# Optimization experiments

Measured on AMD Instinct MI355X. Metric: run time of the kernel, lower is better.

The kernel has to match this reference:

```python
import jax, jax.numpy as jnp
import numpy as np

B, QL, CTX, H = 1, 2048, 2048, 4096
NH, NKV, HD = 32, 8, 128


def rotate_half(x):
    x1, x2 = jnp.split(x, 2, axis=-1)
    return jnp.concatenate([-x2, x1], axis=-1)


def apply_rotary(x, cos, sin):
    # x: [B, h, S, HD]; cos/sin: [B, S, HD] -> broadcast over heads
    cos = cos[:, None, :, :]
    sin = sin[:, None, :, :]
    return x * cos + rotate_half(x) * sin


def setup_inputs() -> dict:
    key = jax.random.key(0)
    ks = jax.random.split(key, 8)
    s = 0.02
    return {
        "hidden_states": jax.random.normal(ks[0], (B, QL, H), jnp.float32),
        "target_hidden": jax.random.normal(ks[1], (B, CTX, H), jnp.float32),
        "cos": jax.random.uniform(ks[2], (B, CTX + QL, HD), jnp.float32),
        "sin": jax.random.uniform(ks[3], (B, CTX + QL, HD), jnp.float32),
        "Wq": jax.random.normal(ks[4], (NH * HD, H), jnp.float32) * s,
        "Wk": jax.random.normal(ks[5], (NKV * HD, H), jnp.float32) * s,
        "Wv": jax.random.normal(ks[6], (NKV * HD, H), jnp.float32) * s,
        "Wo": jax.random.normal(ks[7], (H, NH * HD), jnp.float32) * s,
    }


def reference(hidden_states, target_hidden, cos, sin, Wq, Wk, Wv, Wo):
    bsz, q_len, _ = hidden_states.shape
    ctx_len = target_hidden.shape[1]

    def proj(x, W, nh):  # [B,S,H] @ W.T -> [B,nh,S,HD]
        y = jnp.einsum("bsh,dh->bsd", x, W)
        return y.reshape(bsz, x.shape[1], nh, HD).transpose(0, 2, 1, 3)

    q = proj(hidden_states, Wq, NH)
    k_ctx = proj(target_hidden, Wk, NKV)
    v_ctx = proj(target_hidden, Wv, NKV)
    k_noise = proj(hidden_states, Wk, NKV)
    v_noise = proj(hidden_states, Wv, NKV)

    cos_n = cos[:, ctx_len:ctx_len + q_len]
    sin_n = sin[:, ctx_len:ctx_len + q_len]
    q = apply_rotary(q, cos_n, sin_n)
    k_noise = apply_rotary(k_noise, cos_n, sin_n)
    k_ctx = apply_rotary(k_ctx, cos[:, :ctx_len], sin[:, :ctx_len])

    k = jnp.concatenate([k_ctx, k_noise], axis=2)  # [B,NKV,CTX+QL,HD]
    v = jnp.concatenate([v_ctx, v_noise], axis=2)

    n_rep = NH // NKV
    k = jnp.repeat(k, n_rep, axis=1)  # repeat_interleave on head dim
    v = jnp.repeat(v, n_rep, axis=1)

    scale = 1.0 / jnp.sqrt(jnp.asarray(HD, q.dtype))
    scores = jnp.einsum("bhqd,bhkd->bhqk", q, k) * scale
    probs = jax.nn.softmax(scores, axis=-1)
    attn = jnp.einsum("bhqk,bhkd->bhqd", probs, v)
    attn = attn.transpose(0, 2, 1, 3).reshape(bsz, q_len, NH * HD)
    return jnp.einsum("bsd,hd->bsh", attn, Wo)
```

## Files before the change

### kernel.cpp

```cpp
#include <hip/hip_runtime.h>

typedef unsigned short u16;
typedef _Float16 f16;
typedef _Float16 f16x4 __attribute__((ext_vector_type(4)));
typedef _Float16 f16x8 __attribute__((ext_vector_type(8)));
typedef float f32x4 __attribute__((ext_vector_type(4)));

#define GLL16(gptr, lptr)                                                        \
  __builtin_amdgcn_global_load_lds(                                              \
      (const __attribute__((address_space(1))) void*)(gptr),                     \
      (__attribute__((address_space(3))) void*)(lptr), 16, 0, 0)

__global__ void cast_all_k(const float* __restrict__ h, const float* __restrict__ t,
                           const float* __restrict__ wq, const float* __restrict__ wk,
                           const float* __restrict__ wv, const float* __restrict__ wo,
                           f16* __restrict__ Xcat, f16* __restrict__ Wqb,
                           f16* __restrict__ Wkvb, f16* __restrict__ Wob) {
  long i = (long)blockIdx.x * 256 + threadIdx.x;
  const float* s; f16* d; long off;
  if (i < 2097152)        { s = h;  d = Xcat;            off = i; }
  else if (i < 4194304)   { s = t;  d = Xcat + 8388608;  off = i - 2097152; }
  else if (i < 8388608)   { s = wq; d = Wqb;             off = i - 4194304; }
  else if (i < 9437184)   { s = wk; d = Wkvb;            off = i - 8388608; }
  else if (i < 10485760)  { s = wv; d = Wkvb + 4194304;  off = i - 9437184; }
  else                    { s = wo; d = Wob;             off = i - 10485760; }
  float4 v = *(const float4*)(s + off * 4);
  f16x4 o;
  o.x = (f16)v.x; o.y = (f16)v.y; o.z = (f16)v.z; o.w = (f16)v.w;
  *(f16x4*)(d + off * 4) = o;
}

template <int MODE>
__global__ __launch_bounds__(512, 2) void gemm8k(
    const f16* __restrict__ Xcat, const f16* __restrict__ Wqb,
    const f16* __restrict__ Wkvb, const float* __restrict__ cosT,
    const float* __restrict__ sinT, f16* __restrict__ Qb, f16* __restrict__ Kb,
    f16* __restrict__ Vt, const f16* __restrict__ Ao,
    const f16* __restrict__ Wob, float* __restrict__ Cp, float qscale) {
  __shared__ __align__(16) f16 lds[65536];
  const int tid = threadIdx.x;
  const int w = tid >> 6, lane = tid & 63;
  const int quad = lane >> 4, l16 = lane & 15;
  const int wm = w >> 1, wn = w & 1;

  int b = (int)blockIdx.x;
  int l = ((b & 7) << 5) | (b >> 3);

  const f16 *A, *B;
  long tM, tN;
  int NT, kbeg;
  bool isQ = false, isV = false;
  float* Cz = nullptr;
  if (MODE == 0) {
    kbeg = 0; NT = 64;
    if (l < 128) {
      A = Xcat; B = Wqb; tM = (long)(l >> 4) * 256; tN = (long)(l & 15) * 256;
      isQ = true;
    } else {
      int l2 = l - 128;
      A = Xcat; B = Wkvb; tM = (long)(l2 >> 3) * 256; tN = (long)(l2 & 7) * 256;
      isV = (tN >= 1024);
    }
  } else {
    int z = l >> 7, r0 = l & 127;
    A = Ao; B = Wob; tM = (long)(r0 >> 4) * 256; tN = (long)(r0 & 15) * 256;
    kbeg = z * 2048; NT = 32; Cz = Cp + (long)z * 8388608;
  }

  const int sr8 = lane >> 3;
  const int cg = (lane & 7) ^ sr8;
  const f16* Ag = A + (tM + 16 * w + sr8) * 4096 + kbeg + cg * 8;
  const f16* Bg = B + (tN + 16 * w + sr8) * 4096 + kbeg + cg * 8;
  const int ldsw = w * 1024;

#define STAGE_A(hf, t, c)                                                      \
  do {                                                                         \
    const f16* g_ = Ag + (long)(t) * 64 + (long)(hf) * (128 * 4096);           \
    f16* d_ = &lds[(c) * 16384 + (hf) * 8192 + ldsw];                          \
    GLL16(g_, d_);                                                             \
    GLL16(g_ + 8 * 4096, d_ + 512);                                            \
  } while (0)
#define STAGE_B(hf, t, c)                                                      \
  do {                                                                         \
    const f16* g_ = Bg + (long)(t) * 64 + (long)(hf) * (128 * 4096);           \
    f16* d_ = &lds[32768 + (c) * 16384 + (hf) * 8192 + ldsw];                  \
    GLL16(g_, d_);                                                             \
    GLL16(g_ + 8 * 4096, d_ + 512);                                            \
  } while (0)

  const int rA = wm * 64 + l16;
  const int rB = wn * 128 + l16;
  const int sw = l16 & 7;
#define LDA(fr, mi, kk, c)                                                     \
  fr = *(const f16x8*)&lds[(c) * 16384 + (rA + (mi) * 16) * 64 +               \
                           (((kk) * 4 + quad) ^ sw) * 8]
#define LDB(fr, ni, kk, c)                                                     \
  fr = *(const f16x8*)&lds[32768 + (c) * 16384 + (rB + (ni) * 16) * 64 +       \
                           (((kk) * 4 + quad) ^ sw) * 8]

#define MFMA16 __builtin_amdgcn_mfma_f32_16x16x32_f16
#define BAR() __builtin_amdgcn_s_barrier()
#define WAITDS()                                                               \
  do {                                                                         \
    asm volatile("s_waitcnt lgkmcnt(0)" ::: "memory");                         \
    __builtin_amdgcn_sched_barrier(0);                                         \
  } while (0)

  f32x4 acc[4][8] = {};
  f16x8 af[2][2], bf0[4][2], bf1[4][2];

  STAGE_B(0, 0, 0); STAGE_B(1, 0, 0); STAGE_A(0, 0, 0); STAGE_A(1, 0, 0);
  STAGE_B(0, 1, 1); STAGE_B(1, 1, 1);
  asm volatile("s_waitcnt vmcnt(4)" ::: "memory");
  BAR();

#define TILE_STEP(t, c)                                                        \
  do {                                                                         \
                                       \
    LDA(af[0][0], 0, 0, c); LDA(af[0][1], 0, 1, c);                            \
    LDA(af[1][0], 1, 0, c); LDA(af[1][1], 1, 1, c);                            \
    LDB(bf0[0][0], 0, 0, c); LDB(bf0[0][1], 0, 1, c);                          \
    LDB(bf0[1][0], 1, 0, c); LDB(bf0[1][1], 1, 1, c);                          \
    LDB(bf0[2][0], 2, 0, c); LDB(bf0[2][1], 2, 1, c);                          \
    LDB(bf0[3][0], 3, 0, c); LDB(bf0[3][1], 3, 1, c);                          \
    if ((t) + 1 < NT) STAGE_A(0, (t) + 1, (c) ^ 1);                            \
    BAR(); WAITDS();                                                           \
    __builtin_amdgcn_s_setprio(1);                                             \
    _Pragma("unroll") for (int mi = 0; mi < 2; ++mi)                           \
        _Pragma("unroll") for (int ni = 0; ni < 4; ++ni) {                     \
      acc[mi][ni] = MFMA16(af[mi][0], bf0[ni][0], acc[mi][ni], 0, 0, 0);       \
      acc[mi][ni] = MFMA16(af[mi][1], bf0[ni][1], acc[mi][ni], 0, 0, 0);       \
    }                                                                          \
    __builtin_amdgcn_s_setprio(0);                                             \
    BAR();                                                                     \
                                       \
    LDB(bf1[0][0], 4, 0, c); LDB(bf1[0][1], 4, 1, c);                          \
    LDB(bf1[1][0], 5, 0, c); LDB(bf1[1][1], 5, 1, c);                          \
    LDB(bf1[2][0], 6, 0, c); LDB(bf1[2][1], 6, 1, c);                          \
    LDB(bf1[3][0], 7, 0, c); LDB(bf1[3][1], 7, 1, c);                          \
    if ((t) + 1 < NT) STAGE_A(1, (t) + 1, (c) ^ 1);                            \
    BAR(); WAITDS();                                                           \
    __builtin_amdgcn_s_setprio(1);                                             \
    _Pragma("unroll") for (int mi = 0; mi < 2; ++mi)                           \
        _Pragma("unroll") for (int ni = 0; ni < 4; ++ni) {                     \
      acc[mi][4 + ni] =                                                        \
          MFMA16(af[mi][0], bf1[ni][0], acc[mi][4 + ni], 0, 0, 0);             \
      acc[mi][4 + ni] =                                                        \
          MFMA16(af[mi][1], bf1[ni][1], acc[mi][4 + ni], 0, 0, 0);             \
    }                                                                          \
    __builtin_amdgcn_s_setprio(0);                                             \
    BAR();                                                                     \
                                       \
    LDA(af[0][0], 2, 0, c); LDA(af[0][1], 2, 1, c);                            \
    LDA(af[1][0], 3, 0, c); LDA(af[1][1], 3, 1, c);                            \
    if ((t) + 2 < NT) STAGE_B(0, (t) + 2, c);                                  \
    BAR(); WAITDS();                                                           \
    __builtin_amdgcn_s_setprio(1);                                             \
    _Pragma("unroll") for (int mi = 0; mi < 2; ++mi)                           \
        _Pragma("unroll") for (int ni = 0; ni < 4; ++ni) {                     \
      acc[2 + mi][ni] = MFMA16(af[mi][0], bf0[ni][0], acc[2 + mi][ni], 0, 0, 0);\
      acc[2 + mi][ni] = MFMA16(af[mi][1], bf0[ni][1], acc[2 + mi][ni], 0, 0, 0);\
    }                                                                          \
    __builtin_amdgcn_s_setprio(0);                                             \
    BAR();                                                                     \
      \
    if ((t) + 2 < NT) STAGE_B(1, (t) + 2, c);                                  \
    BAR();                                                                     \
    __builtin_amdgcn_s_setprio(1);                                             \
    _Pragma("unroll") for (int mi = 0; mi < 2; ++mi)                           \
        _Pragma("unroll") for (int ni = 0; ni < 4; ++ni) {                     \
      acc[2 + mi][4 + ni] =                                                    \
          MFMA16(af[mi][0], bf1[ni][0], acc[2 + mi][4 + ni], 0, 0, 0);         \
      acc[2 + mi][4 + ni] =                                                    \
          MFMA16(af[mi][1], bf1[ni][1], acc[2 + mi][4 + ni], 0, 0, 0);         \
    }                                                                          \
    __builtin_amdgcn_s_setprio(0);                                             \
    if ((t) + 2 < NT)                                                          \
      asm volatile("s_waitcnt vmcnt(4)" ::: "memory");                         \
    else                                                                       \
      asm volatile("s_waitcnt vmcnt(0)" ::: "memory");                         \
    BAR();                                                                     \
  } while (0)

  for (int t = 0; t < NT; t += 2) {
    TILE_STEP(t, 0);
    TILE_STEP(t + 1, 1);
  }

  if (MODE == 1) {
#pragma unroll
    for (int mi = 0; mi < 4; ++mi)
#pragma unroll
      for (int ni = 0; ni < 8; ++ni)
#pragma unroll
        for (int r = 0; r < 4; ++r) {
          long row = tM + wm * 64 + mi * 16 + quad * 4 + r;
          long col = tN + wn * 128 + ni * 16 + l16;
          Cz[row * 4096 + col] = acc[mi][ni][r];
        }
  } else if (isV) {
    const int kvh = (int)((tN - 1024) >> 7) + wn;
#pragma unroll
    for (int mi = 0; mi < 4; ++mi) {
      int key0 = ((int)tM + wm * 64 + mi * 16 + quad * 4) ^ 2048;
#pragma unroll
      for (int ni = 0; ni < 8; ++ni) {
        int d = ni * 16 + l16;
        f16x4 pk;
#pragma unroll
        for (int r = 0; r < 4; ++r) pk[r] = (f16)acc[mi][ni][r];
        *(f16x4*)&Vt[((long)kvh * 128 + d) * 4096 + key0] = pk;
      }
    }
  } else {
    const float sc = isQ ? qscale : 1.0f;
    const int h = (int)(tN >> 7) + wn;
#pragma unroll
    for (int mi = 0; mi < 4; ++mi)
#pragma unroll
      for (int r = 0; r < 4; ++r) {
        int rg = (int)tM + wm * 64 + mi * 16 + quad * 4 + r;
        int pos = isQ ? (2048 + rg) : (rg ^ 2048);
        const float* cp = cosT + (long)pos * 128;
        const float* sp = sinT + (long)pos * 128;
        f16* orow = isQ ? Qb + ((long)h * 2048 + rg) * 128
                        : Kb + ((long)h * 4096 + pos) * 128;
#pragma unroll
        for (int ni = 0; ni < 4; ++ni) {
          int d = ni * 16 + l16;
          float x0 = acc[mi][ni][r], x1 = acc[mi][ni + 4][r];
          orow[d] = (f16)((x0 * cp[d] - x1 * sp[d]) * sc);
          orow[d + 64] = (f16)((x1 * cp[d + 64] + x0 * sp[d + 64]) * sc);
        }
      }
  }
#undef TILE_STEP
#undef STAGE_A
#undef STAGE_B
#undef LDA
#undef LDB
#undef WAITDS
#undef BAR
#undef MFMA16
}

__global__ __launch_bounds__(256, 2) void flash_k(const f16* __restrict__ Qb,
                                                  const f16* __restrict__ Kb,
                                                  const f16* __restrict__ Vt,
                                                  f16* __restrict__ Ob) {
  __shared__ __align__(16) f16 Ks[2][64 * 128];
  __shared__ __align__(16) f16 Vs[128 * 64];
  __shared__ __align__(16) f16 Ps[4][32 * 72];
  const int tid = threadIdx.x;
  const int w = tid >> 6, lane = tid & 63;
  const int quad = lane >> 4, l16 = lane & 15;
  const int b = blockIdx.x;
  const int kvh = b & 7;
  const int j = b >> 3;
  const int h = kvh * 4 + (j >> 4);
  const int q0 = (j & 15) * 128;

  f16x8 qf[2][4];
#pragma unroll
  for (int mi = 0; mi < 2; ++mi) {
    const f16* qrow = Qb + ((long)h * 2048 + q0 + w * 32 + mi * 16 + l16) * 128 + quad * 8;
#pragma unroll
    for (int kc = 0; kc < 4; ++kc) qf[mi][kc] = *(const f16x8*)(qrow + kc * 32);
  }

  f32x4 of[2][8] = {};
  float lsum[2] = {0.f, 0.f};
  const f16* Kg = Kb + (long)kvh * 4096 * 128;
  const f16* Vg = Vt + (long)kvh * 128 * 4096;
  f16* PsW = &Ps[w][0];

  const int krow = (lane >> 4);
  const int kslot = lane & 15;
  const int vrow = (lane >> 3);
  const int vslot = lane & 7;
  const int vgc = vslot ^ (vrow & 7);

#define FBAR() __builtin_amdgcn_s_barrier()
#define STAGE_K(kt_, c_)                                                       \
  do {                                                                         \
    _Pragma("unroll") for (int it = 0; it < 4; ++it) {                         \
      int row = w * 16 + it * 4 + krow;                                        \
      int gc = kslot ^ (it * 4 + krow);                                        \
      GLL16(Kg + (long)((kt_)*64 + row) * 128 + gc * 8,                        \
            &Ks[c_][(w * 16 + it * 4) * 128]);                                 \
    }                                                                          \
  } while (0)
#define STAGE_V(kt_)                                                           \
  do {                                                                         \
    _Pragma("unroll") for (int it = 0; it < 4; ++it) {                         \
      int row = w * 32 + it * 8 + vrow;                                        \
      GLL16(Vg + (long)row * 4096 + (kt_)*64 + vgc * 8,                        \
            &Vs[(w * 32 + it * 8) * 64]);                                      \
    }                                                                          \
  } while (0)

  STAGE_K(0, 0);

  for (int kt = 0; kt < 64; ++kt) {
    const int c = kt & 1;
    FBAR();
    STAGE_V(kt);
    asm volatile("s_waitcnt vmcnt(4)" ::: "memory");
    FBAR();
    __builtin_amdgcn_sched_barrier(0);

    f32x4 s[2][4] = {};
    __builtin_amdgcn_s_setprio(1);
#pragma unroll
    for (int nt = 0; nt < 4; ++nt) {
      f16x8 ak[4];
#pragma unroll
      for (int kc = 0; kc < 4; ++kc) {
        int slot = (kc * 4 + quad) ^ l16;
        ak[kc] = *(const f16x8*)&Ks[c][(nt * 16 + l16) * 128 + slot * 8];
      }
#pragma unroll
      for (int mi = 0; mi < 2; ++mi)
#pragma unroll
        for (int kc = 0; kc < 4; ++kc)
          s[mi][nt] = __builtin_amdgcn_mfma_f32_16x16x32_f16(ak[kc], qf[mi][kc],
                                                             s[mi][nt], 0, 0, 0);
    }
    __builtin_amdgcn_s_setprio(0);

    if (kt < 63) STAGE_K(kt + 1, c ^ 1);

#pragma unroll
    for (int mi = 0; mi < 2; ++mi)
#pragma unroll
      for (int nt = 0; nt < 4; ++nt) {
        f16x4 pk;
#pragma unroll
        for (int r = 0; r < 4; ++r) {
          float pv = __builtin_amdgcn_exp2f(s[mi][nt][r]);
          lsum[mi] += pv;
          pk[r] = (f16)pv;
        }
        *(f16x4*)&PsW[(mi * 16 + l16) * 72 + nt * 16 + quad * 4] = pk;
      }

    if (kt < 63)
      asm volatile("s_waitcnt vmcnt(4)" ::: "memory");
    else
      asm volatile("s_waitcnt vmcnt(0)" ::: "memory");
    FBAR();
    __builtin_amdgcn_sched_barrier(0);

    __builtin_amdgcn_s_setprio(1);
#pragma unroll
    for (int kc2 = 0; kc2 < 2; ++kc2) {
      f16x8 bp[2];
#pragma unroll
      for (int mi = 0; mi < 2; ++mi)
        bp[mi] = *(const f16x8*)&PsW[(mi * 16 + l16) * 72 + kc2 * 32 + quad * 8];
#pragma unroll
      for (int dt = 0; dt < 8; ++dt) {
        int slot = (kc2 * 4 + quad) ^ (l16 & 7);
        f16x8 av = *(const f16x8*)&Vs[(dt * 16 + l16) * 64 + slot * 8];
#pragma unroll
        for (int mi = 0; mi < 2; ++mi)
          of[mi][dt] =
              __builtin_amdgcn_mfma_f32_16x16x32_f16(av, bp[mi], of[mi][dt], 0, 0, 0);
      }
    }
    __builtin_amdgcn_s_setprio(0);
  }
#undef STAGE_K
#undef STAGE_V
#undef FBAR

#pragma unroll
  for (int mi = 0; mi < 2; ++mi) {
    float v = lsum[mi];
    v += __shfl_xor(v, 16, 64);
    v += __shfl_xor(v, 32, 64);
    float inv = 1.0f / v;
    long q = q0 + w * 32 + mi * 16 + l16;
#pragma unroll
    for (int dt = 0; dt < 8; ++dt) {
      f16x4 o4;
#pragma unroll
      for (int r = 0; r < 4; ++r) o4[r] = (f16)(of[mi][dt][r] * inv);
      *(f16x4*)&Ob[q * 4096 + h * 128 + dt * 16 + quad * 4] = o4;
    }
  }
}

__global__ void reduce2_k(const float* __restrict__ p, float* __restrict__ out) {
  long i = ((long)blockIdx.x * 256 + threadIdx.x) * 4;
  float4 a = *(const float4*)(p + i);
  float4 b = *(const float4*)(p + 8388608 + i);
  a.x += b.x; a.y += b.y; a.z += b.z; a.w += b.w;
  *(float4*)(out + i) = a;
}

extern "C" void kernel_launch(void* const* d_in, const int* in_sizes, int n_in,
                              void* d_out, int out_size, void* d_ws, size_t ws_size,
                              hipStream_t stream) {
  (void)in_sizes; (void)n_in; (void)out_size; (void)ws_size;
  const float* hidden = (const float*)d_in[0];
  const float* target = (const float*)d_in[1];
  const float* cosT = (const float*)d_in[2];
  const float* sinT = (const float*)d_in[3];
  const float* Wq = (const float*)d_in[4];
  const float* Wk = (const float*)d_in[5];
  const float* Wv = (const float*)d_in[6];
  const float* Wo = (const float*)d_in[7];
  float* out = (float*)d_out;

  char* p = (char*)d_ws;
  auto alloc = [&](size_t bytes) {
    char* r = p;
    p += (bytes + 255) & ~(size_t)255;
    return r;
  };
  f16* Xcat = (f16*)alloc(4096ull * 4096 * 2);
  f16* Wqb  = (f16*)alloc(4096ull * 4096 * 2);
  f16* Wkvb = (f16*)alloc(2048ull * 4096 * 2);
  f16* Wob  = (f16*)alloc(4096ull * 4096 * 2);
  f16* Qb   = (f16*)alloc(32ull * 2048 * 128 * 2);
  f16* Kb   = (f16*)alloc(8ull * 4096 * 128 * 2);
  f16* Vt   = (f16*)alloc(8ull * 128 * 4096 * 2);
  f16* Ao   = (f16*)alloc(2048ull * 4096 * 2);
  float* Pp = (float*)d_ws;

  cast_all_k<<<57344, 256, 0, stream>>>(hidden, target, Wq, Wk, Wv, Wo,
                                        Xcat, Wqb, Wkvb, Wob);

  const float QSC = (float)(0.08838834764831845 * 1.4426950408889634);
  gemm8k<0><<<256, 512, 0, stream>>>(Xcat, Wqb, Wkvb, cosT, sinT, Qb, Kb, Vt,
                                     nullptr, nullptr, nullptr, QSC);

  flash_k<<<512, 256, 0, stream>>>(Qb, Kb, Vt, Ao);

  gemm8k<1><<<256, 512, 0, stream>>>(nullptr, nullptr, nullptr, nullptr, nullptr,
                                     nullptr, nullptr, nullptr, Ao, Wob, Pp, 0.f);
  reduce2_k<<<8192, 256, 0, stream>>>(Pp, out);
}
```

Measured before the change: 582.7 us.

## Software-pipeline attention loop: overlap next QK^T MFMAs with current softmax exp

Restructures the flash-attention inner loop so the QK^T scores for tile kt are computed while the exp/P-store of tile kt-1 runs, with a prologue and epilogue handling the first and last tiles. The goal is to interleave MFMA work with exp2 VALU work so neither unit idles, and to reschedule the V staging after PV accumulation. It raises register pressure by holding two score tiles, drops the sched_barriers, and changes the order of LDS hazards and waitcnts, which could cause stalls or spills.

```diff
diff --git a/kernel.cpp b/kernel.cpp
--- a/kernel.cpp
+++ b/kernel.cpp
@@ -299,79 +299,108 @@
     }                                                                          \
   } while (0)
 
+#define QKT(dst, c_)                                                           \
+  do {                                                                         \
+    _Pragma("unroll") for (int nt = 0; nt < 4; ++nt) {                         \
+      f16x8 ak[4];                                                             \
+      _Pragma("unroll") for (int kc = 0; kc < 4; ++kc) {                       \
+        int slot = (kc * 4 + quad) ^ l16;                                      \
+        ak[kc] = *(const f16x8*)&Ks[c_][(nt * 16 + l16) * 128 + slot * 8];     \
+      }                                                                        \
+      _Pragma("unroll") for (int mi = 0; mi < 2; ++mi)                         \
+          _Pragma("unroll") for (int kc = 0; kc < 4; ++kc)                     \
+        dst[mi][nt] = __builtin_amdgcn_mfma_f32_16x16x32_f16(                  \
+            ak[kc], qf[mi][kc], dst[mi][nt], 0, 0, 0);                         \
+    }                                                                          \
+  } while (0)
+
+#define EXPP(src)                                                              \
+  do {                                                                         \
+    _Pragma("unroll") for (int mi = 0; mi < 2; ++mi)                           \
+        _Pragma("unroll") for (int nt = 0; nt < 4; ++nt) {                     \
+      f16x4 pk;                                                                \
+      _Pragma("unroll") for (int r = 0; r < 4; ++r) {                          \
+        float pv = __builtin_amdgcn_exp2f(src[mi][nt][r]);                     \
+        lsum[mi] += pv;                                                        \
+        pk[r] = (f16)pv;                                                       \
+      }                                                                        \
+      *(f16x4*)&PsW[(mi * 16 + l16) * 72 + nt * 16 + quad * 4] = pk;           \
+    }                                                                          \
+  } while (0)
+
+#define PVACC()                                                                \
+  do {                                                                         \
+    _Pragma("unroll") for (int kc2 = 0; kc2 < 2; ++kc2) {                      \
+      f16x8 bp[2];                                                             \
+      _Pragma("unroll") for (int mi = 0; mi < 2; ++mi)                         \
+        bp[mi] = *(const f16x8*)&PsW[(mi * 16 + l16) * 72 + kc2 * 32 +         \
+                                     quad * 8];                                \
+      _Pragma("unroll") for (int dt = 0; dt < 8; ++dt) {                       \
+        int slot = (kc2 * 4 + quad) ^ (l16 & 7);                               \
+        f16x8 av = *(const f16x8*)&Vs[(dt * 16 + l16) * 64 + slot * 8];        \
+        _Pragma("unroll") for (int mi = 0; mi < 2; ++mi)                       \
+          of[mi][dt] = __builtin_amdgcn_mfma_f32_16x16x32_f16(                 \
+              av, bp[mi], of[mi][dt], 0, 0, 0);                                \
+      }                                                                        \
+    }                                                                          \
+  } while (0)
+
+  f32x4 sP[2][4] = {};
+  f32x4 sC[2][4];
+
   STAGE_K(0, 0);
-
-  for (int kt = 0; kt < 64; ++kt) {
+  asm volatile("s_waitcnt vmcnt(0)" ::: "memory");
+  FBAR();
+  __builtin_amdgcn_s_setprio(1);
+  QKT(sP, 0);
+  __builtin_amdgcn_s_setprio(0);
+  STAGE_K(1, 1);
+  STAGE_V(0);
+
+  for (int kt = 1; kt < 64; ++kt) {
     const int c = kt & 1;
-    FBAR();
-    STAGE_V(kt);
     asm volatile("s_waitcnt vmcnt(4)" ::: "memory");
     FBAR();
-    __builtin_amdgcn_sched_barrier(0);
-
-    f32x4 s[2][4] = {};
+
+#pragma unroll
+    for (int mi = 0; mi < 2; ++mi)
+#pragma unroll
+      for (int nt = 0; nt < 4; ++nt) sC[mi][nt] = f32x4{0.f, 0.f, 0.f, 0.f};
     __builtin_amdgcn_s_setprio(1);
-#pragma unroll
-    for (int nt = 0; nt < 4; ++nt) {
-      f16x8 ak[4];
-#pragma unroll
-      for (int kc = 0; kc < 4; ++kc) {
-        int slot = (kc * 4 + quad) ^ l16;
-        ak[kc] = *(const f16x8*)&Ks[c][(nt * 16 + l16) * 128 + slot * 8];
-      }
-#pragma unroll
-      for (int mi = 0; mi < 2; ++mi)
-#pragma unroll
-        for (int kc = 0; kc < 4; ++kc)
-          s[mi][nt] = __builtin_amdgcn_mfma_f32_16x16x32_f16(ak[kc], qf[mi][kc],
-                                                             s[mi][nt], 0, 0, 0);
-    }
+    QKT(sC, c);
+    EXPP(sP);
     __builtin_amdgcn_s_setprio(0);
 
     if (kt < 63) STAGE_K(kt + 1, c ^ 1);
-
-#pragma unroll
-    for (int mi = 0; mi < 2; ++mi)
-#pragma unroll
-      for (int nt = 0; nt < 4; ++nt) {
-        f16x4 pk;
-#pragma unroll
-        for (int r = 0; r < 4; ++r) {
-          float pv = __builtin_amdgcn_exp2f(s[mi][nt][r]);
-          lsum[mi] += pv;
-          pk[r] = (f16)pv;
-        }
-        *(f16x4*)&PsW[(mi * 16 + l16) * 72 + nt * 16 + quad * 4] = pk;
-      }
-
     if (kt < 63)
       asm volatile("s_waitcnt vmcnt(4)" ::: "memory");
     else
       asm volatile("s_waitcnt vmcnt(0)" ::: "memory");
     FBAR();
-    __builtin_amdgcn_sched_barrier(0);
 
     __builtin_amdgcn_s_setprio(1);
-#pragma unroll
-    for (int kc2 = 0; kc2 < 2; ++kc2) {
-      f16x8 bp[2];
-#pragma unroll
-      for (int mi = 0; mi < 2; ++mi)
-        bp[mi] = *(const f16x8*)&PsW[(mi * 16 + l16) * 72 + kc2 * 32 + quad * 8];
-#pragma unroll
-      for (int dt = 0; dt < 8; ++dt) {
-        int slot = (kc2 * 4 + quad) ^ (l16 & 7);
-        f16x8 av = *(const f16x8*)&Vs[(dt * 16 + l16) * 64 + slot * 8];
-#pragma unroll
-        for (int mi = 0; mi < 2; ++mi)
-          of[mi][dt] =
-              __builtin_amdgcn_mfma_f32_16x16x32_f16(av, bp[mi], of[mi][dt], 0, 0, 0);
-      }
-    }
+    PVACC();
     __builtin_amdgcn_s_setprio(0);
-  }
+
+    FBAR();
+    STAGE_V(kt);
+
+#pragma unroll
+    for (int mi = 0; mi < 2; ++mi)
+#pragma unroll
+      for (int nt = 0; nt < 4; ++nt) sP[mi][nt] = sC[mi][nt];
+  }
+
+  EXPP(sP);
+  asm volatile("s_waitcnt vmcnt(0)" ::: "memory");
+  FBAR();
+  PVACC();
+
 #undef STAGE_K
 #undef STAGE_V
+#undef QKT
+#undef EXPP
+#undef PVACC
 #undef FBAR
 
 #pragma unroll
```

After: 583.1 us. About the same (+0.1%).
